# Optimization experiments

Measured on AMD Instinct MI355X. Metric: run time of the kernel, lower is better.

Reference implementation:

```python
import jax, jax.numpy as jnp
import numpy as np

N_NODES = 50000
N_EDGES = 800000
D_IN = 96
D_OUT = 96
NEG_SLOPE = 0.2


def setup_inputs() -> dict:
    key = jax.random.key(0)
    k1, k2, k3, k4, k5 = jax.random.split(key, 5)
    x = jax.random.normal(k1, (N_NODES, D_IN), dtype=jnp.float32)
    W = jax.random.normal(k2, (D_IN, D_OUT), dtype=jnp.float32) * (1.0 / np.sqrt(D_IN))
    att_src = jax.random.normal(k3, (D_OUT,), dtype=jnp.float32) * 0.1
    att_dst = jax.random.normal(k4, (D_OUT,), dtype=jnp.float32) * 0.1
    bias = jnp.zeros((D_OUT,), dtype=jnp.float32)
    edge_index = jax.random.randint(k5, (2, N_EDGES), 0, N_NODES, dtype=jnp.int64)
    return {"x": x, "W": W, "att_src": att_src, "att_dst": att_dst,
            "bias": bias, "edge_index": edge_index}


def reference(x, W, att_src, att_dst, bias, edge_index):
    N = x.shape[0]
    # Linear transform: h = x W   [N, D_out]
    h = x @ W
    # PyG GATConv default add_self_loops=True
    loops = jnp.arange(N, dtype=edge_index.dtype)
    src = jnp.concatenate([edge_index[0], loops])  # message source j
    dst = jnp.concatenate([edge_index[1], loops])  # aggregation target i
    # Per-node attention halves, gathered per edge
    a_src = h @ att_src  # [N]
    a_dst = h @ att_dst  # [N]
    e = jax.nn.leaky_relu(a_src[src] + a_dst[dst], NEG_SLOPE)  # [E+N]
    # Segment softmax over edges sharing the same destination
    m = jax.ops.segment_max(e, dst, num_segments=N)  # every node has a self-loop
    e = jnp.exp(e - m[dst])
    denom = jax.ops.segment_sum(e, dst, num_segments=N)
    alpha = e / (denom[dst] + 1e-16)  # [E+N]
    # Weighted scatter-aggregate of source features
    out = jax.ops.segment_sum(h[src] * alpha[:, None], dst, num_segments=N)
    return jnp.tanh(out + bias)
```

## Files before the change

kernel.cpp:

```cpp
#include <hip/hip_runtime.h>
#include <hip/hip_bf16.h>
#include <cstdint>

#define N_NODES 50000
#define N_EDGES 800000
#define D 96
#define NEG_SLOPE 0.2f
#define R1ROWS 16
#define BUCKET 64
#define NXCD 8
#define DST_PER_PART (N_NODES / NXCD)

__global__ __launch_bounds__(384) void k0_proj(
    const float* __restrict__ W, const float* __restrict__ att_src,
    const float* __restrict__ att_dst, float* __restrict__ p_src,
    float* __restrict__ p_dst) {
    __shared__ float Wl[D * (D + 1)];
    __shared__ float asl[D], adl[D];
    __shared__ float rs[4][D], rd[4][D];
    const int tx = threadIdx.x, ty = threadIdx.y;
    const int t = ty * 96 + tx;
    for (int i = t; i < D * D; i += 384) Wl[(i / D) * (D + 1) + (i % D)] = W[i];
    if (t < D) { asl[t] = att_src[t]; adl[t] = att_dst[t]; }
    __syncthreads();
    float ps = 0.f, pd = 0.f;
    const float* wrow = &Wl[tx * (D + 1) + ty * 24];
#pragma unroll
    for (int c = 0; c < 24; ++c) {
        float w = wrow[c];
        ps += w * asl[ty * 24 + c];
        pd += w * adl[ty * 24 + c];
    }
    rs[ty][tx] = ps; rd[ty][tx] = pd;
    __syncthreads();
    if (ty == 0) {
        p_src[tx] = rs[0][tx] + rs[1][tx] + rs[2][tx] + rs[3][tx];
        p_dst[tx] = rd[0][tx] + rd[1][tx] + rd[2][tx] + rd[3][tx];
    }
}

__global__ __launch_bounds__(384) void k1_gemm(
    const float* __restrict__ x, const float* __restrict__ W,
    __hip_bfloat16* __restrict__ hb) {
    __shared__ float Ws[D][D];
    __shared__ float xs[R1ROWS][D];
    const int tx = threadIdx.x, ty = threadIdx.y;
    const int t = ty * 96 + tx;
    const size_t row0 = (size_t)blockIdx.x * R1ROWS;

    {
        const float4* W4 = (const float4*)W;
        float4* Ws4 = (float4*)Ws;
#pragma unroll
        for (int i = 0; i < 6; ++i) Ws4[t + 384 * i] = W4[t + 384 * i];
        const float4* x4 = (const float4*)(x + row0 * D);
        ((float4*)xs)[t] = x4[t];
    }
    __syncthreads();

    float acc0 = 0.f, acc1 = 0.f, acc2 = 0.f, acc3 = 0.f;
#pragma unroll
    for (int k = 0; k < D; k += 4) {
        float4 xa = *(const float4*)&xs[ty][k];
        float4 xb = *(const float4*)&xs[ty + 4][k];
        float4 xc = *(const float4*)&xs[ty + 8][k];
        float4 xd = *(const float4*)&xs[ty + 12][k];
        float w0 = Ws[k][tx], w1 = Ws[k + 1][tx], w2 = Ws[k + 2][tx], w3 = Ws[k + 3][tx];
        acc0 += xa.x * w0 + xa.y * w1 + xa.z * w2 + xa.w * w3;
        acc1 += xb.x * w0 + xb.y * w1 + xb.z * w2 + xb.w * w3;
        acc2 += xc.x * w0 + xc.y * w1 + xc.z * w2 + xc.w * w3;
        acc3 += xd.x * w0 + xd.y * w1 + xd.z * w2 + xd.w * w3;
    }
    hb[(row0 + ty     ) * D + tx] = __float2bfloat16(acc0);
    hb[(row0 + ty + 4 ) * D + tx] = __float2bfloat16(acc1);
    hb[(row0 + ty + 8 ) * D + tx] = __float2bfloat16(acc2);
    hb[(row0 + ty + 12) * D + tx] = __float2bfloat16(acc3);
}

__global__ __launch_bounds__(256) void k1b_att(
    const float* __restrict__ x, const float* __restrict__ p_src,
    const float* __restrict__ p_dst, float* __restrict__ a_src,
    float* __restrict__ a_dst, int* __restrict__ cnt) {
    const int lane = threadIdx.x & 63;
    const int row = (blockIdx.x * 256 + threadIdx.x) >> 6;
    if (row >= N_NODES) return;
    float s = 0.f, d = 0.f;
    if (lane < 48) {
        float2 xv = *(const float2*)(x + (size_t)row * D + lane * 2);
        float2 ps = *(const float2*)(p_src + lane * 2);
        float2 pd = *(const float2*)(p_dst + lane * 2);
        s = xv.x * ps.x + xv.y * ps.y;
        d = xv.x * pd.x + xv.y * pd.y;
    }
#pragma unroll
    for (int off = 32; off >= 1; off >>= 1) {
        s += __shfl_down(s, off);
        d += __shfl_down(d, off);
    }
    if (lane == 0) { a_src[row] = s; a_dst[row] = d; cnt[row] = 0; }
}

__global__ void k_bucket(const int* __restrict__ ei,
                         const float* __restrict__ a_src, const float* __restrict__ a_dst,
                         int* __restrict__ cnt, uint* __restrict__ bkt) {
    const int part = blockIdx.x & (NXCD - 1);
    const int e = (blockIdx.x >> 3) * 256 + threadIdx.x;
    if (e >= N_EDGES) return;
    int d = ei[N_EDGES + e];
    int lo = part * DST_PER_PART;
    if (d < lo || d >= lo + DST_PER_PART) return;
    int s = ei[e];
    float v = a_src[s] + a_dst[d];
    v = v > 0.f ? v : NEG_SLOPE * v;
    float w = __expf(v);
    uint u = __float_as_uint(w);
    uint wb = (u + 0x7FFFu + ((u >> 16) & 1u)) & 0xFFFF0000u;
    uint pk = wb | (uint)s;
    int pos = atomicAdd(&cnt[d], 1);
    if (pos < BUCKET) bkt[(size_t)d * BUCKET + pos] = pk;
}

__global__ __launch_bounds__(256) void k_gather(
    const int* __restrict__ cnt, const uint* __restrict__ bkt,
    const float* __restrict__ a_src, const float* __restrict__ a_dst,
    const __hip_bfloat16* __restrict__ hb, const float* __restrict__ bias,
    float* __restrict__ out) {
    const uint lane = threadIdx.x & 63;
    const int node = (blockIdx.x * 256 + threadIdx.x) >> 6;
    if (node >= N_NODES) return;
    const uint* __restrict__ hbu = (const uint*)hb;
    const uint* __restrict__ bucket = bkt + (size_t)node * BUCKET;
    const int cn = min(cnt[node], BUCKET);

    float es = a_src[node] + a_dst[node];
    es = es > 0.f ? es : NEG_SLOPE * es;
    float wself = __expf(es);
    uint pself = hbu[(uint)node * 48u + lane];
    float acc0 = __uint_as_float(pself << 16) * wself;
    float acc1 = __uint_as_float(pself & 0xffff0000u) * wself;
    float wsum = wself;

    int k = 0;
    for (; k + 15 < cn; k += 16) {
        uint b[16];
        *(uint4*)&b[0]  = *(const uint4*)&bucket[k];
        *(uint4*)&b[4]  = *(const uint4*)&bucket[k + 4];
        *(uint4*)&b[8]  = *(const uint4*)&bucket[k + 8];
        *(uint4*)&b[12] = *(const uint4*)&bucket[k + 12];
        uint p[16];
#pragma unroll
        for (int j = 0; j < 16; ++j) p[j] = hbu[(b[j] & 0xFFFFu) * 48u + lane];
#pragma unroll
        for (int j = 0; j < 16; ++j) {
            float w = __uint_as_float(b[j] & 0xFFFF0000u);
            acc0 += __uint_as_float(p[j] << 16) * w;
            acc1 += __uint_as_float(p[j] & 0xffff0000u) * w;
            wsum += w;
        }
    }
    if (k + 7 < cn) {
        uint b[8];
        *(uint4*)&b[0] = *(const uint4*)&bucket[k];
        *(uint4*)&b[4] = *(const uint4*)&bucket[k + 4];
        uint p[8];
#pragma unroll
        for (int j = 0; j < 8; ++j) p[j] = hbu[(b[j] & 0xFFFFu) * 48u + lane];
#pragma unroll
        for (int j = 0; j < 8; ++j) {
            float w = __uint_as_float(b[j] & 0xFFFF0000u);
            acc0 += __uint_as_float(p[j] << 16) * w;
            acc1 += __uint_as_float(p[j] & 0xffff0000u) * w;
            wsum += w;
        }
        k += 8;
    }
    if (k + 3 < cn) {
        uint b[4];
        *(uint4*)&b[0] = *(const uint4*)&bucket[k];
        uint p[4];
#pragma unroll
        for (int j = 0; j < 4; ++j) p[j] = hbu[(b[j] & 0xFFFFu) * 48u + lane];
#pragma unroll
        for (int j = 0; j < 4; ++j) {
            float w = __uint_as_float(b[j] & 0xFFFF0000u);
            acc0 += __uint_as_float(p[j] << 16) * w;
            acc1 += __uint_as_float(p[j] & 0xffff0000u) * w;
            wsum += w;
        }
        k += 4;
    }
    for (; k < cn; ++k) {
        uint e0 = bucket[k];
        uint p0 = hbu[(e0 & 0xFFFFu) * 48u + lane];
        float w0 = __uint_as_float(e0 & 0xFFFF0000u);
        acc0 += __uint_as_float(p0 << 16) * w0;
        acc1 += __uint_as_float(p0 & 0xffff0000u) * w0;
        wsum += w0;
    }

    if (lane < 48) {
        float inv = 1.f / (wsum + 1e-16f);
        float2 bv = *(const float2*)(bias + lane * 2);
        float2 o;
        o.x = tanhf(acc0 * inv + bv.x);
        o.y = tanhf(acc1 * inv + bv.y);
        *(float2*)(out + (size_t)node * D + lane * 2) = o;
    }
}

extern "C" void kernel_launch(void* const* d_in, const int* in_sizes, int n_in,
                              void* d_out, int out_size, void* d_ws, size_t ws_size,
                              hipStream_t stream) {
    const float* x       = (const float*)d_in[0];
    const float* W       = (const float*)d_in[1];
    const float* att_src = (const float*)d_in[2];
    const float* att_dst = (const float*)d_in[3];
    const float* bias    = (const float*)d_in[4];
    const int*   ei      = (const int*)d_in[5];
    float* out = (float*)d_out;

    char* ws = (char*)d_ws;
    __hip_bfloat16* hb = (__hip_bfloat16*)ws; ws += (size_t)N_NODES * D * 2;
    float* a_src  = (float*)ws; ws += (size_t)N_NODES * 4;
    float* a_dst  = (float*)ws; ws += (size_t)N_NODES * 4;
    int*   cnt    = (int*)ws;   ws += (size_t)N_NODES * 4;
    float* p_src  = (float*)ws; ws += (size_t)D * 4;
    float* p_dst  = (float*)ws; ws += (size_t)D * 4;
    uint*  bkt    = (uint*)ws;  ws += (size_t)N_NODES * BUCKET * 4;

    k0_proj<<<1, dim3(96, 4), 0, stream>>>(W, att_src, att_dst, p_src, p_dst);
    k1b_att<<<(N_NODES * 64 + 255) / 256, 256, 0, stream>>>(x, p_src, p_dst, a_src, a_dst, cnt);
    k_bucket<<<((N_EDGES + 255) / 256) * NXCD, 256, 0, stream>>>(ei, a_src, a_dst, cnt, bkt);
    k1_gemm<<<N_NODES / R1ROWS, dim3(96, 4), 0, stream>>>(x, W, hb);
    k_gather<<<(N_NODES * 64 + 255) / 256, 256, 0, stream>>>(cnt, bkt, a_src, a_dst, hb, bias, out);
}
```

Baseline: 120.6 us.

## Fuse projection, attention logits and GEMM into one kernel; XCD-partition gather

Merges the W·att projection, per-node attention logits and the bf16 GEMM into a single kernel. Each block recomputes the W·att projection from its shared W tile and computes a_src/a_dst for its 16 rows from the padded x tile, which drops two launches and a second read of x. The gather kernel now maps blocks to destination partitions interleaved by XCD, matching the bucket kernel, so bucket and count data written on one XCD should be read from the same L2. The cost is redundant per-block projection work and a serialized 32-thread logit step at the end of each block.

```diff
diff --git a/kernel.cpp b/kernel.cpp
--- a/kernel.cpp
+++ b/kernel.cpp
@@ -7,43 +7,20 @@
 #define D 96
 #define NEG_SLOPE 0.2f
 #define R1ROWS 16
+#define XPAD 100
 #define BUCKET 64
 #define NXCD 8
 #define DST_PER_PART (N_NODES / NXCD)
 
-__global__ __launch_bounds__(384) void k0_proj(
-    const float* __restrict__ W, const float* __restrict__ att_src,
-    const float* __restrict__ att_dst, float* __restrict__ p_src,
-    float* __restrict__ p_dst) {
-    __shared__ float Wl[D * (D + 1)];
+__global__ __launch_bounds__(384) void k1_all(
+    const float* __restrict__ x, const float* __restrict__ W,
+    const float* __restrict__ att_src, const float* __restrict__ att_dst,
+    __hip_bfloat16* __restrict__ hb, float* __restrict__ a_src,
+    float* __restrict__ a_dst, int* __restrict__ cnt) {
+    __shared__ float Ws[D][D];
+    __shared__ float xs[R1ROWS][XPAD];
     __shared__ float asl[D], adl[D];
-    __shared__ float rs[4][D], rd[4][D];
-    const int tx = threadIdx.x, ty = threadIdx.y;
-    const int t = ty * 96 + tx;
-    for (int i = t; i < D * D; i += 384) Wl[(i / D) * (D + 1) + (i % D)] = W[i];
-    if (t < D) { asl[t] = att_src[t]; adl[t] = att_dst[t]; }
-    __syncthreads();
-    float ps = 0.f, pd = 0.f;
-    const float* wrow = &Wl[tx * (D + 1) + ty * 24];
-#pragma unroll
-    for (int c = 0; c < 24; ++c) {
-        float w = wrow[c];
-        ps += w * asl[ty * 24 + c];
-        pd += w * adl[ty * 24 + c];
-    }
-    rs[ty][tx] = ps; rd[ty][tx] = pd;
-    __syncthreads();
-    if (ty == 0) {
-        p_src[tx] = rs[0][tx] + rs[1][tx] + rs[2][tx] + rs[3][tx];
-        p_dst[tx] = rd[0][tx] + rd[1][tx] + rd[2][tx] + rd[3][tx];
-    }
-}
-
-__global__ __launch_bounds__(384) void k1_gemm(
-    const float* __restrict__ x, const float* __restrict__ W,
-    __hip_bfloat16* __restrict__ hb) {
-    __shared__ float Ws[D][D];
-    __shared__ float xs[R1ROWS][D];
+    __shared__ float ps[D], pd[D];
     const int tx = threadIdx.x, ty = threadIdx.y;
     const int t = ty * 96 + tx;
     const size_t row0 = (size_t)blockIdx.x * R1ROWS;
@@ -54,7 +31,27 @@
 #pragma unroll
         for (int i = 0; i < 6; ++i) Ws4[t + 384 * i] = W4[t + 384 * i];
         const float4* x4 = (const float4*)(x + row0 * D);
-        ((float4*)xs)[t] = x4[t];
+        float4 v = x4[t];
+        int idx4 = t * 4;
+        *(float4*)&xs[idx4 / D][idx4 % D] = v;
+        if (t < D) { asl[t] = att_src[t]; adl[t] = att_dst[t]; }
+    }
+    __syncthreads();
+
+    if (ty == 0) {
+        float acc = 0.f;
+        for (int cc = 0; cc < D; ++cc) {
+            int c = cc + tx; if (c >= D) c -= D;
+            acc += Ws[tx][c] * asl[c];
+        }
+        ps[tx] = acc;
+    } else if (ty == 1) {
+        float acc = 0.f;
+        for (int cc = 0; cc < D; ++cc) {
+            int c = cc + tx; if (c >= D) c -= D;
+            acc += Ws[tx][c] * adl[c];
+        }
+        pd[tx] = acc;
     }
     __syncthreads();
 
@@ -75,29 +72,24 @@
     hb[(row0 + ty + 4 ) * D + tx] = __float2bfloat16(acc1);
     hb[(row0 + ty + 8 ) * D + tx] = __float2bfloat16(acc2);
     hb[(row0 + ty + 12) * D + tx] = __float2bfloat16(acc3);
-}
-
-__global__ __launch_bounds__(256) void k1b_att(
-    const float* __restrict__ x, const float* __restrict__ p_src,
-    const float* __restrict__ p_dst, float* __restrict__ a_src,
-    float* __restrict__ a_dst, int* __restrict__ cnt) {
-    const int lane = threadIdx.x & 63;
-    const int row = (blockIdx.x * 256 + threadIdx.x) >> 6;
-    if (row >= N_NODES) return;
-    float s = 0.f, d = 0.f;
-    if (lane < 48) {
-        float2 xv = *(const float2*)(x + (size_t)row * D + lane * 2);
-        float2 ps = *(const float2*)(p_src + lane * 2);
-        float2 pd = *(const float2*)(p_dst + lane * 2);
-        s = xv.x * ps.x + xv.y * ps.y;
-        d = xv.x * pd.x + xv.y * pd.y;
-    }
-#pragma unroll
-    for (int off = 32; off >= 1; off >>= 1) {
-        s += __shfl_down(s, off);
-        d += __shfl_down(d, off);
-    }
-    if (lane == 0) { a_src[row] = s; a_dst[row] = d; cnt[row] = 0; }
+
+    if (t < 32) {
+        const int r = t & 15;
+        const int k0 = (t >> 4) * 48;
+        float s = 0.f, d = 0.f;
+        for (int i = 0; i < 48; ++i) {
+            float xv = xs[r][k0 + i];
+            s += xv * ps[k0 + i];
+            d += xv * pd[k0 + i];
+        }
+        s += __shfl_down(s, 16);
+        d += __shfl_down(d, 16);
+        if (t < 16) {
+            a_src[row0 + r] = s;
+            a_dst[row0 + r] = d;
+            cnt[row0 + r] = 0;
+        }
+    }
 }
 
 __global__ void k_bucket(const int* __restrict__ ei,
@@ -126,8 +118,10 @@
     const __hip_bfloat16* __restrict__ hb, const float* __restrict__ bias,
     float* __restrict__ out) {
     const uint lane = threadIdx.x & 63;
-    const int node = (blockIdx.x * 256 + threadIdx.x) >> 6;
-    if (node >= N_NODES) return;
+    const int part = blockIdx.x & (NXCD - 1);
+    const int l = (int)((blockIdx.x >> 3) * 4 + (threadIdx.x >> 6));
+    if (l >= DST_PER_PART) return;
+    const int node = part * DST_PER_PART + l;
     const uint* __restrict__ hbu = (const uint*)hb;
     const uint* __restrict__ bucket = bkt + (size_t)node * BUCKET;
     const int cn = min(cnt[node], BUCKET);
@@ -224,13 +218,11 @@
     float* a_src  = (float*)ws; ws += (size_t)N_NODES * 4;
     float* a_dst  = (float*)ws; ws += (size_t)N_NODES * 4;
     int*   cnt    = (int*)ws;   ws += (size_t)N_NODES * 4;
-    float* p_src  = (float*)ws; ws += (size_t)D * 4;
-    float* p_dst  = (float*)ws; ws += (size_t)D * 4;
     uint*  bkt    = (uint*)ws;  ws += (size_t)N_NODES * BUCKET * 4;
 
-    k0_proj<<<1, dim3(96, 4), 0, stream>>>(W, att_src, att_dst, p_src, p_dst);
-    k1b_att<<<(N_NODES * 64 + 255) / 256, 256, 0, stream>>>(x, p_src, p_dst, a_src, a_dst, cnt);
+    k1_all<<<N_NODES / R1ROWS, dim3(96, 4), 0, stream>>>(
+        x, W, att_src, att_dst, hb, a_src, a_dst, cnt);
     k_bucket<<<((N_EDGES + 255) / 256) * NXCD, 256, 0, stream>>>(ei, a_src, a_dst, cnt, bkt);
-    k1_gemm<<<N_NODES / R1ROWS, dim3(96, 4), 0, stream>>>(x, W, hb);
-    k_gather<<<(N_NODES * 64 + 255) / 256, 256, 0, stream>>>(cnt, bkt, a_src, a_dst, hb, bias, out);
-}
+    k_gather<<<((DST_PER_PART + 3) / 4) * NXCD, 256, 0, stream>>>(
+        cnt, bkt, a_src, a_dst, hb, bias, out);
+}
```

Result: slower. 133.4 us (+10.6%).

## Compute attention logits from fp32 h and partition gather by XCD

Applied to the files above, without the earlier changes.

Removes the W·att projection kernel. The GEMM now writes an fp32 copy of h into the output buffer, and the attention kernel reads it to compute a_src/a_dst directly, so the GEMM moves ahead of bucketing. The gather kernel's node mapping is also interleaved by XCD partition, aiming to match the bucket partitioning for L2 locality. The trade-off is an extra 19 MB fp32 write plus a read of it, in exchange for one fewer launch and a different node-to-block order.

```diff
diff --git a/kernel.cpp b/kernel.cpp
--- a/kernel.cpp
+++ b/kernel.cpp
@@ -11,37 +11,9 @@
 #define NXCD 8
 #define DST_PER_PART (N_NODES / NXCD)
 
-__global__ __launch_bounds__(384) void k0_proj(
-    const float* __restrict__ W, const float* __restrict__ att_src,
-    const float* __restrict__ att_dst, float* __restrict__ p_src,
-    float* __restrict__ p_dst) {
-    __shared__ float Wl[D * (D + 1)];
-    __shared__ float asl[D], adl[D];
-    __shared__ float rs[4][D], rd[4][D];
-    const int tx = threadIdx.x, ty = threadIdx.y;
-    const int t = ty * 96 + tx;
-    for (int i = t; i < D * D; i += 384) Wl[(i / D) * (D + 1) + (i % D)] = W[i];
-    if (t < D) { asl[t] = att_src[t]; adl[t] = att_dst[t]; }
-    __syncthreads();
-    float ps = 0.f, pd = 0.f;
-    const float* wrow = &Wl[tx * (D + 1) + ty * 24];
-#pragma unroll
-    for (int c = 0; c < 24; ++c) {
-        float w = wrow[c];
-        ps += w * asl[ty * 24 + c];
-        pd += w * adl[ty * 24 + c];
-    }
-    rs[ty][tx] = ps; rd[ty][tx] = pd;
-    __syncthreads();
-    if (ty == 0) {
-        p_src[tx] = rs[0][tx] + rs[1][tx] + rs[2][tx] + rs[3][tx];
-        p_dst[tx] = rd[0][tx] + rd[1][tx] + rd[2][tx] + rd[3][tx];
-    }
-}
-
 __global__ __launch_bounds__(384) void k1_gemm(
     const float* __restrict__ x, const float* __restrict__ W,
-    __hip_bfloat16* __restrict__ hb) {
+    float* __restrict__ hf, __hip_bfloat16* __restrict__ hb) {
     __shared__ float Ws[D][D];
     __shared__ float xs[R1ROWS][D];
     const int tx = threadIdx.x, ty = threadIdx.y;
@@ -71,6 +43,10 @@
         acc2 += xc.x * w0 + xc.y * w1 + xc.z * w2 + xc.w * w3;
         acc3 += xd.x * w0 + xd.y * w1 + xd.z * w2 + xd.w * w3;
     }
+    hf[(row0 + ty     ) * D + tx] = acc0;
+    hf[(row0 + ty + 4 ) * D + tx] = acc1;
+    hf[(row0 + ty + 8 ) * D + tx] = acc2;
+    hf[(row0 + ty + 12) * D + tx] = acc3;
     hb[(row0 + ty     ) * D + tx] = __float2bfloat16(acc0);
     hb[(row0 + ty + 4 ) * D + tx] = __float2bfloat16(acc1);
     hb[(row0 + ty + 8 ) * D + tx] = __float2bfloat16(acc2);
@@ -78,19 +54,19 @@
 }
 
 __global__ __launch_bounds__(256) void k1b_att(
-    const float* __restrict__ x, const float* __restrict__ p_src,
-    const float* __restrict__ p_dst, float* __restrict__ a_src,
+    const float* __restrict__ hf, const float* __restrict__ att_src,
+    const float* __restrict__ att_dst, float* __restrict__ a_src,
     float* __restrict__ a_dst, int* __restrict__ cnt) {
     const int lane = threadIdx.x & 63;
     const int row = (blockIdx.x * 256 + threadIdx.x) >> 6;
     if (row >= N_NODES) return;
     float s = 0.f, d = 0.f;
     if (lane < 48) {
-        float2 xv = *(const float2*)(x + (size_t)row * D + lane * 2);
-        float2 ps = *(const float2*)(p_src + lane * 2);
-        float2 pd = *(const float2*)(p_dst + lane * 2);
-        s = xv.x * ps.x + xv.y * ps.y;
-        d = xv.x * pd.x + xv.y * pd.y;
+        float2 hv = *(const float2*)(hf + (size_t)row * D + lane * 2);
+        float2 as = *(const float2*)(att_src + lane * 2);
+        float2 ad = *(const float2*)(att_dst + lane * 2);
+        s = hv.x * as.x + hv.y * as.y;
+        d = hv.x * ad.x + hv.y * ad.y;
     }
 #pragma unroll
     for (int off = 32; off >= 1; off >>= 1) {
@@ -126,8 +102,10 @@
     const __hip_bfloat16* __restrict__ hb, const float* __restrict__ bias,
     float* __restrict__ out) {
     const uint lane = threadIdx.x & 63;
-    const int node = (blockIdx.x * 256 + threadIdx.x) >> 6;
-    if (node >= N_NODES) return;
+    const int part = blockIdx.x & (NXCD - 1);
+    const int l = (int)((blockIdx.x >> 3) * 4 + (threadIdx.x >> 6));
+    if (l >= DST_PER_PART) return;
+    const int node = part * DST_PER_PART + l;
     const uint* __restrict__ hbu = (const uint*)hb;
     const uint* __restrict__ bucket = bkt + (size_t)node * BUCKET;
     const int cn = min(cnt[node], BUCKET);
@@ -219,18 +197,18 @@
     const int*   ei      = (const int*)d_in[5];
     float* out = (float*)d_out;
 
+    float* hf = out;
+
     char* ws = (char*)d_ws;
     __hip_bfloat16* hb = (__hip_bfloat16*)ws; ws += (size_t)N_NODES * D * 2;
     float* a_src  = (float*)ws; ws += (size_t)N_NODES * 4;
     float* a_dst  = (float*)ws; ws += (size_t)N_NODES * 4;
     int*   cnt    = (int*)ws;   ws += (size_t)N_NODES * 4;
-    float* p_src  = (float*)ws; ws += (size_t)D * 4;
-    float* p_dst  = (float*)ws; ws += (size_t)D * 4;
     uint*  bkt    = (uint*)ws;  ws += (size_t)N_NODES * BUCKET * 4;
 
-    k0_proj<<<1, dim3(96, 4), 0, stream>>>(W, att_src, att_dst, p_src, p_dst);
-    k1b_att<<<(N_NODES * 64 + 255) / 256, 256, 0, stream>>>(x, p_src, p_dst, a_src, a_dst, cnt);
+    k1_gemm<<<N_NODES / R1ROWS, dim3(96, 4), 0, stream>>>(x, W, hf, hb);
+    k1b_att<<<(N_NODES * 64 + 255) / 256, 256, 0, stream>>>(hf, att_src, att_dst, a_src, a_dst, cnt);
     k_bucket<<<((N_EDGES + 255) / 256) * NXCD, 256, 0, stream>>>(ei, a_src, a_dst, cnt, bkt);
-    k1_gemm<<<N_NODES / R1ROWS, dim3(96, 4), 0, stream>>>(x, W, hb);
-    k_gather<<<(N_NODES * 64 + 255) / 256, 256, 0, stream>>>(cnt, bkt, a_src, a_dst, hb, bias, out);
-}
+    k_gather<<<((DST_PER_PART + 3) / 4) * NXCD, 256, 0, stream>>>(
+        cnt, bkt, a_src, a_dst, hb, bias, out);
+}
```

Result: faster. 115.6 us (-4.1%).
